# Kernel tuning notes

Hardware: AMD Instinct MI355X
Metric: run time of the kernel (lower is better)

The kernel has to match this reference:

```python
import jax, jax.numpy as jnp
import numpy as np

BN_EPS = 1e-5


def setup_inputs() -> dict:
    key = jax.random.key(0)
    ks = jax.random.split(key, 4)
    B, N, D = 8, 8192, 256
    outD = 256
    s = 1.0 / np.sqrt(D)
    return {
        "feature": jax.random.normal(ks[0], (B, N, D), dtype=jnp.float32),
        "W_qk": jax.random.normal(ks[1], (2, D, D), dtype=jnp.float32) * s,
        "b_qk": jnp.zeros((2, D), dtype=jnp.float32),
        "W_v": jax.random.normal(ks[2], (D, outD), dtype=jnp.float32) * s,
        "b_v": jnp.zeros((outD,), dtype=jnp.float32),
        "gamma": jnp.ones((D,), dtype=jnp.float32),
        "beta": jnp.zeros((D,), dtype=jnp.float32),
    }


def reference(feature, W_qk, b_qk, W_v, b_v, gamma, beta):
    # QK: [B, 2, N, D]
    QK = jnp.einsum("bnd,kde->bkne", feature, W_qk) + b_qk[None, :, None, :]
    # value: [B, N, outD]
    value = jnp.einsum("bnd,de->bne", feature, W_v) + b_v
    query = QK[:, 0]  # [B, N, D]
    key = QK[:, 1]    # [B, N, D]
    # softmax over the sequence axis (dim=1), per (batch, channel)
    sm = jax.nn.softmax(key, axis=1)
    # lambda context: softmax^T @ value -> [B, D, outD]
    lam = jnp.einsum("bnd,bne->bde", sm, value)
    # BatchNorm1d(featureDim) in training mode: channel axis = D (axis 1),
    # stats over (batch, spatial) = axes (0, 2); biased variance as torch uses.
    mean = jnp.mean(lam, axis=(0, 2), keepdims=True)
    var = jnp.var(lam, axis=(0, 2), keepdims=True)
    bn = (lam - mean) * jax.lax.rsqrt(var + BN_EPS)
    bn = bn * gamma[None, :, None] + beta[None, :, None]
    # result: query @ BN -> [B, N, outD]
    return jnp.einsum("bnd,bde->bne", query, bn)
```

## Files before the change

### kernel.cpp

```cpp
#include <hip/hip_runtime.h>

typedef unsigned short u16;
typedef __bf16 bf16x8 __attribute__((ext_vector_type(8)));
typedef float f32x4 __attribute__((ext_vector_type(4)));

#define LOG2E 1.44269504088896f

__device__ inline u16 f2b(float f) {
    unsigned u = __float_as_uint(f);
    u += 0x7fff + ((u >> 16) & 1);
    return (u16)(u >> 16);
}
__device__ inline float b2f(u16 u) { return __uint_as_float(((unsigned)u) << 16); }
__device__ inline unsigned pk2(float a, float b) {
    return (unsigned)f2b(a) | ((unsigned)f2b(b) << 16);
}
__device__ inline uint4 pack8(float4 a, float4 b) {
    return uint4{pk2(a.x, a.y), pk2(a.z, a.w), pk2(b.x, b.y), pk2(b.z, b.w)};
}
__device__ inline f32x4 mfma_bf16(uint4 a, uint4 b, f32x4 c) {
    return __builtin_amdgcn_mfma_f32_16x16x32_bf16(
        __builtin_bit_cast(bf16x8, a), __builtin_bit_cast(bf16x8, b), c, 0, 0, 0);
}
__device__ inline void ld16(const u16* g, u16* l) {
    __builtin_amdgcn_global_load_lds(
        (const __attribute__((address_space(1))) unsigned int*)g,
        (__attribute__((address_space(3))) unsigned int*)l, 16, 0, 0);
}
__device__ inline uint4 expfrag(uint4 v, float nc) {
    float e[8];
#pragma unroll
    for (int i = 0; i < 4; ++i) {
        unsigned u = ((const unsigned*)&v)[i];
        e[2 * i] = exp2f(fmaf(b2f((u16)(u & 0xffff)), LOG2E, nc));
        e[2 * i + 1] = exp2f(fmaf(b2f((u16)(u >> 16)), LOG2E, nc));
    }
    uint4 r;
    asm("v_cvt_pk_bf16_f32 %0, %1, %2" : "=v"(r.x) : "v"(e[0]), "v"(e[1]));
    asm("v_cvt_pk_bf16_f32 %0, %1, %2" : "=v"(r.y) : "v"(e[2]), "v"(e[3]));
    asm("v_cvt_pk_bf16_f32 %0, %1, %2" : "=v"(r.z) : "v"(e[4]), "v"(e[5]));
    asm("v_cvt_pk_bf16_f32 %0, %1, %2" : "=v"(r.w) : "v"(e[6]), "v"(e[7]));
    return r;
}


__global__ __launch_bounds__(256) void prep_w(const float* __restrict__ Wqk,
                                              const float* __restrict__ Wv,
                                              u16* __restrict__ WkT,
                                              u16* __restrict__ WvT,
                                              u16* __restrict__ Wqb) {
    int idx = blockIdx.x * 256 + threadIdx.x;
    int which = idx >> 16;
    int i = (idx >> 8) & 255;
    int j = idx & 255;
    if (which == 0)
        WkT[i * 256 + j] = f2b(Wqk[65536 + j * 256 + i]);
    else if (which == 1)
        WvT[i * 256 + j] = f2b(Wv[j * 256 + i]);
    else
        Wqb[i * 256 + j] = f2b(Wqk[i * 256 + j]);
}

__global__ __launch_bounds__(256, 2) void gemm_kv(const float* __restrict__ A,
                                                  const u16* __restrict__ BtK,
                                                  const u16* __restrict__ BtV,
                                                  const float* __restrict__ biasK,
                                                  const float* __restrict__ biasV,
                                                  u16* __restrict__ KT,
                                                  u16* __restrict__ VT,
                                                  float* __restrict__ partial) {
    __shared__ __align__(16) u16 lds[36864];

    const int t = threadIdx.x;
    const int r0 = blockIdx.x * 64;
    const int w = t >> 6, lane = t & 63, l15 = lane & 15, q = lane >> 4;
    const int sq = ((lane & 3) ^ ((lane >> 3) & 3)) * 8;
    const int qs = (q ^ ((l15 >> 1) & 3)) * 8;
    const int awoff = (t >> 2) * 32 + sq;
    const int brr = t >> 2;

    f32x4 accK[4][4], accV[4][4];
#pragma unroll
    for (int rt = 0; rt < 4; ++rt)
#pragma unroll
        for (int ct = 0; ct < 4; ++ct) {
            accK[rt][ct] = f32x4{0.f, 0.f, 0.f, 0.f};
            accV[rt][ct] = f32x4{0.f, 0.f, 0.f, 0.f};
        }

    const float* Arow = A + (long)(r0 + brr) * 256 + (t & 3) * 8;
    float4 p0 = ((const float4*)Arow)[0], p1 = ((const float4*)Arow)[1];
    float4 c0_ = *(const float4*)(Arow + 32), c1_ = *(const float4*)(Arow + 36);
    float4 d0_ = *(const float4*)(Arow + 64), d1_ = *(const float4*)(Arow + 68);

    {
        u16* dK = lds + 4096 + w * 512;
#pragma unroll
        for (int j = 0; j < 4; ++j) {
            int br = j * 64 + brr;
            ld16(BtK + br * 256 + sq, dK + j * 2048);
            ld16(BtV + br * 256 + sq, dK + 8192 + j * 2048);
        }
    }
    *(uint4*)(lds + awoff) = pack8(p0, p1);
    __syncthreads();

#pragma unroll
    for (int t8 = 0; t8 < 8; ++t8) {
        const int cur = t8 & 1;
        if (t8 < 7) {
            const int k0 = (t8 + 1) * 32;
            u16* dK = lds + 4096 + (cur ^ 1) * 16384 + w * 512;
#pragma unroll
            for (int j = 0; j < 4; ++j) {
                int br = j * 64 + brr;
                ld16(BtK + br * 256 + k0 + sq, dK + j * 2048);
                ld16(BtV + br * 256 + k0 + sq, dK + 8192 + j * 2048);
            }
            *(uint4*)(lds + (cur ^ 1) * 2048 + awoff) = pack8(c0_, c1_);
            c0_ = d0_; c1_ = d1_;
            if (t8 < 5) {
                d0_ = *(const float4*)(Arow + (t8 + 3) * 32);
                d1_ = *(const float4*)(Arow + (t8 + 3) * 32 + 4);
            }
        }
        const u16* Asc = lds + cur * 2048;
        const u16* Bc = lds + 4096 + cur * 16384;
        uint4 af[4];
#pragma unroll
        for (int rt = 0; rt < 4; ++rt)
            af[rt] = *(const uint4*)(Asc + (rt * 16 + l15) * 32 + qs);
#pragma unroll
        for (int ct = 0; ct < 4; ++ct) {
            const int bo = (w * 64 + ct * 16 + l15) * 32 + qs;
            uint4 bK = *(const uint4*)(Bc + bo);
            uint4 bV = *(const uint4*)(Bc + 8192 + bo);
#pragma unroll
            for (int rt = 0; rt < 4; ++rt) {
                accK[rt][ct] = mfma_bf16(af[rt], bK, accK[rt][ct]);
                accV[rt][ct] = mfma_bf16(af[rt], bV, accV[rt][ct]);
            }
        }
        __syncthreads();
    }

    const int bb = r0 >> 13;
    const int nt0 = (r0 & 8191) >> 5;
    const int nch = nt0 >> 1;
    u16* Ct = lds;
#pragma unroll
    for (int pass = 0; pass < 2; ++pass) {
        const f32x4(*acc)[4] = pass ? accV : accK;
        const float* bias = pass ? biasV : biasK;
        u16* CT = pass ? VT : KT;
#pragma unroll
        for (int ct = 0; ct < 4; ++ct) {
            const int col = w * 64 + ct * 16 + l15;
            const float bv = bias[col];
            ushort4 pks[4];
#pragma unroll
            for (int rt = 0; rt < 4; ++rt) {
                ushort4 pk;
                pk.x = f2b(acc[rt][ct][0] + bv);
                pk.y = f2b(acc[rt][ct][1] + bv);
                pk.z = f2b(acc[rt][ct][2] + bv);
                pk.w = f2b(acc[rt][ct][3] + bv);
                pks[rt] = pk;
                *(ushort4*)&Ct[col * 72 + rt * 16 + q * 4] = pk;
            }
            if (pass == 0) {
                float zm = -1e30f;
#pragma unroll
                for (int rt = 0; rt < 4; ++rt)
                    zm = fmaxf(zm,
                               fmaxf(fmaxf(b2f(pks[rt].x), b2f(pks[rt].y)),
                                     fmaxf(b2f(pks[rt].z), b2f(pks[rt].w))));
                zm = fmaxf(zm, __shfl_xor(zm, 16, 64));
                zm = fmaxf(zm, __shfl_xor(zm, 32, 64));
                zm *= LOG2E;
                float zs = 0.f;
#pragma unroll
                for (int rt = 0; rt < 4; ++rt) {
                    zs += exp2f(fmaf(b2f(pks[rt].x), LOG2E, -zm));
                    zs += exp2f(fmaf(b2f(pks[rt].y), LOG2E, -zm));
                    zs += exp2f(fmaf(b2f(pks[rt].z), LOG2E, -zm));
                    zs += exp2f(fmaf(b2f(pks[rt].w), LOG2E, -zm));
                }
                zs += __shfl_xor(zs, 16, 64);
                zs += __shfl_xor(zs, 32, 64);
                if (q == 0) {
                    float* pp =
                        partial + (((long)(bb * 128 + nch)) * 256 + col) * 2;
                    pp[0] = zm;
                    pp[1] = zs;
                }
            }
        }
        __syncthreads();
        {
            const long tb = (((long)(bb * 256 + nt0)) * 256 + t) * 32;
#pragma unroll
            for (int j2 = 0; j2 < 2; ++j2)
#pragma unroll
                for (int g = 0; g < 4; ++g)
                    *(uint4*)(CT + tb + j2 * 8192 + g * 8) =
                        *(const uint4*)&Ct[t * 72 + j2 * 32 + g * 8];
        }
        __syncthreads();
    }
}

__global__ __launch_bounds__(256) void stats2(const float* __restrict__ partial,
                                              float* __restrict__ ctab) {
    const int b = blockIdx.x, dg = blockIdx.y;
    const int t = threadIdx.x;
    const int d = dg * 32 + (t & 31);
    const int ci = t >> 5;
    float m = -1e30f, sum = 0.f;
#pragma unroll 4
    for (int k = 0; k < 16; ++k) {
        int i = ci * 16 + k;
        const float* pp = partial + (((long)(b * 128 + i)) * 256 + d) * 2;
        float mi = pp[0], si = pp[1];
        float M = fmaxf(m, mi);
        sum = sum * exp2f(m - M) + si * exp2f(mi - M);
        m = M;
    }
    __shared__ float red[512];
    red[t] = m;
    red[t + 256] = sum;
    __syncthreads();
    if (ci == 0) {
#pragma unroll
        for (int j = 1; j < 8; ++j) {
            float mi = red[t + j * 32], si = red[t + 256 + j * 32];
            float M = fmaxf(m, mi);
            sum = sum * exp2f(m - M) + si * exp2f(mi - M);
            m = M;
        }
        ctab[b * 256 + d] = m + log2f(sum);
    }
}

__global__ __launch_bounds__(256, 3) void gemm_out(const float* __restrict__ A,
                                                   const u16* __restrict__ WfoldT,
                                                   const float* __restrict__ outb,
                                                   float* __restrict__ C) {
    __shared__ __align__(16) u16 lds[20480];
    const int t = threadIdx.x;
    const int r0 = blockIdx.x * 64;
    const int bb = r0 >> 13;
    const int w = t >> 6, lane = t & 63, l15 = lane & 15, q = lane >> 4;
    const int sq = ((lane & 3) ^ ((lane >> 3) & 3)) * 8;
    const int qs = (q ^ ((l15 >> 1) & 3)) * 8;
    const int awoff = (t >> 2) * 32 + sq;
    const int brr = t >> 2;
    const u16* Bt = WfoldT + (long)bb * 65536;

    f32x4 acc[4][4];
#pragma unroll
    for (int rt = 0; rt < 4; ++rt)
#pragma unroll
        for (int ct = 0; ct < 4; ++ct) acc[rt][ct] = f32x4{0.f, 0.f, 0.f, 0.f};

    const float* Arow = A + (long)(r0 + brr) * 256 + (t & 3) * 8;
    float4 p0 = ((const float4*)Arow)[0], p1 = ((const float4*)Arow)[1];
    float4 c0_ = *(const float4*)(Arow + 32), c1_ = *(const float4*)(Arow + 36);
    float4 d0_ = *(const float4*)(Arow + 64), d1_ = *(const float4*)(Arow + 68);

    {
        u16* dB = lds + 4096 + w * 512;
#pragma unroll
        for (int j = 0; j < 4; ++j)
            ld16(Bt + (j * 64 + brr) * 256 + sq, dB + j * 2048);
    }
    *(uint4*)(lds + awoff) = pack8(p0, p1);
    __syncthreads();

#pragma unroll
    for (int t8 = 0; t8 < 8; ++t8) {
        const int cur = t8 & 1;
        if (t8 < 7) {
            const int k0 = (t8 + 1) * 32;
            u16* dB = lds + 4096 + (cur ^ 1) * 8192 + w * 512;
#pragma unroll
            for (int j = 0; j < 4; ++j)
                ld16(Bt + (j * 64 + brr) * 256 + k0 + sq, dB + j * 2048);
            *(uint4*)(lds + (cur ^ 1) * 2048 + awoff) = pack8(c0_, c1_);
            c0_ = d0_; c1_ = d1_;
            if (t8 < 5) {
                d0_ = *(const float4*)(Arow + (t8 + 3) * 32);
                d1_ = *(const float4*)(Arow + (t8 + 3) * 32 + 4);
            }
        }
        const u16* Asc = lds + cur * 2048;
        const u16* Bc = lds + 4096 + cur * 8192;
        uint4 af[4];
#pragma unroll
        for (int rt = 0; rt < 4; ++rt)
            af[rt] = *(const uint4*)(Asc + (rt * 16 + l15) * 32 + qs);
#pragma unroll
        for (int ct = 0; ct < 4; ++ct) {
            uint4 bf = *(const uint4*)(Bc + (w * 64 + ct * 16 + l15) * 32 + qs);
#pragma unroll
            for (int rt = 0; rt < 4; ++rt)
                acc[rt][ct] = mfma_bf16(af[rt], bf, acc[rt][ct]);
        }
        __syncthreads();
    }

#pragma unroll
    for (int ct = 0; ct < 4; ++ct) {
        const int col = w * 64 + ct * 16 + l15;
        const float bv = outb[bb * 256 + col];
#pragma unroll
        for (int rt = 0; rt < 4; ++rt) {
            const long rbase = r0 + rt * 16 + q * 4;
#pragma unroll
            for (int r = 0; r < 4; ++r)
                C[(rbase + r) * 256 + col] = acc[rt][ct][r] + bv;
        }
    }
}

__global__ __launch_bounds__(512, 2) void gemm_lam(const u16* __restrict__ VT,
                                                   const u16* __restrict__ KT,
                                                   const float* __restrict__ ctab,
                                                   float* __restrict__ lamP,
                                                   int nk) {
    __shared__ __align__(16) u16 lds[32768];
    const int t = threadIdx.x;
    const int b = blockIdx.x;
    const int s = blockIdx.y;
    const int w = t >> 6, lane = t & 63, l15 = lane & 15, q = lane >> 4;
    const int eg = w >> 2, dg = w & 3;
    const int sq = ((lane & 3) ^ ((lane >> 3) & 3)) * 8;
    const int qs = (q ^ ((l15 >> 1) & 3)) * 8;

    const int nt0 = s * nk;
    const u16* Vb = VT + ((long)(b * 256 + nt0)) * 8192;
    const u16* Kb = KT + ((long)(b * 256 + nt0)) * 8192;

    float nc[4];
#pragma unroll
    for (int ct = 0; ct < 4; ++ct)
        nc[ct] = -ctab[b * 256 + dg * 64 + ct * 16 + l15];

    f32x4 acc[8][4];
#pragma unroll
    for (int rt = 0; rt < 8; ++rt)
#pragma unroll
        for (int ct = 0; ct < 4; ++ct) acc[rt][ct] = f32x4{0.f, 0.f, 0.f, 0.f};

#define STAGE_TILE(tile, buf)                                                  \
    {                                                                          \
        _Pragma("unroll") for (int j = 0; j < 2; ++j) {                        \
            int g = j * 512 + t;                                               \
            ld16((tile) + (g >> 2) * 32 + sq, (buf) + (j * 512 + w * 64) * 8); \
        }                                                                      \
    }

    STAGE_TILE(Vb, lds)
    STAGE_TILE(Kb, lds + 8192)
    __syncthreads();

    for (int ks = 0; ks < nk; ++ks) {
        const int cur = ks & 1;
        if (ks + 1 < nk) {
            const u16* Vn = Vb + (long)(ks + 1) * 8192;
            const u16* Kn = Kb + (long)(ks + 1) * 8192;
            u16* dst = lds + (cur ^ 1) * 16384;
            STAGE_TILE(Vn, dst)
            STAGE_TILE(Kn, dst + 8192)
        }
        const u16* Vs = lds + cur * 16384;
        const u16* Ks = Vs + 8192;
        uint4 bf[4];
#pragma unroll
        for (int ct = 0; ct < 4; ++ct)
            bf[ct] = expfrag(
                *(const uint4*)(Ks + (dg * 64 + ct * 16 + l15) * 32 + qs),
                nc[ct]);
#pragma unroll
        for (int rt = 0; rt < 8; ++rt) {
            uint4 af = *(const uint4*)(Vs + (eg * 128 + rt * 16 + l15) * 32 + qs);
#pragma unroll
            for (int ct = 0; ct < 4; ++ct)
                acc[rt][ct] = mfma_bf16(af, bf[ct], acc[rt][ct]);
        }
        __syncthreads();
    }
#undef STAGE_TILE

    float* outp = lamP + (long)s * 524288 + (long)b * 65536;
#pragma unroll
    for (int rt = 0; rt < 8; ++rt)
#pragma unroll
        for (int ct = 0; ct < 4; ++ct) {
            const int col = dg * 64 + ct * 16 + l15;
            const int row = eg * 128 + rt * 16 + q * 4;
#pragma unroll
            for (int r = 0; r < 4; ++r)
                outp[(long)(row + r) * 256 + col] = acc[rt][ct][r];
        }
}

__global__ __launch_bounds__(256) void reduce_lam(const float* __restrict__ lamP,
                                                  float* __restrict__ lamT, int S) {
    int i = blockIdx.x * 256 + threadIdx.x;
    float4 v = ((const float4*)lamP)[i];
    for (int s = 1; s < S; ++s) {
        float4 p = ((const float4*)(lamP + (long)s * 524288))[i];
        v.x += p.x; v.y += p.y; v.z += p.z; v.w += p.w;
    }
    ((float4*)lamT)[i] = v;
}

__global__ __launch_bounds__(256, 4) void gemm_fold(const u16* __restrict__ Abn,
                                                    const u16* __restrict__ Wqb,
                                                    u16* __restrict__ WfoldT) {
    __shared__ __align__(16) u16 lds[4096];
    u16* As = lds;
    u16* Bs = lds + 2048;

    const int t = threadIdx.x;
    const int r0 = blockIdx.x * 64;
    const int c0 = blockIdx.y * 64;
    const int w = t >> 6, lane = t & 63, l15 = lane & 15, q = lane >> 4;

    f32x4 acc[4];
#pragma unroll
    for (int c = 0; c < 4; ++c) acc[c] = f32x4{0.f, 0.f, 0.f, 0.f};

    const int br = t >> 2;
    const int bk = (t & 3) * 8;

    for (int k0 = 0; k0 < 256; k0 += 32) {
        ld16(Abn + (long)(r0 + br) * 256 + k0 + bk, As + w * 512);
        ld16(Wqb + (long)(c0 + br) * 256 + k0 + bk, Bs + w * 512);
        __syncthreads();
        uint4 af = *(const uint4*)(As + (w * 16 + l15) * 32 + q * 8);
#pragma unroll
        for (int c = 0; c < 4; ++c) {
            uint4 bf = *(const uint4*)(Bs + (c * 16 + l15) * 32 + q * 8);
            acc[c] = mfma_bf16(af, bf, acc[c]);
        }
        __syncthreads();
    }

#pragma unroll
    for (int c = 0; c < 4; ++c) {
        int col = c0 + c * 16 + l15;
#pragma unroll
        for (int r = 0; r < 4; ++r) {
            int row = r0 + w * 16 + q * 4 + r;
            WfoldT[(long)row * 256 + col] = f2b(acc[c][r]);
        }
    }
}

__global__ __launch_bounds__(256) void bn_kernel(const float* __restrict__ lamT,
                                                 const float* __restrict__ gamma,
                                                 const float* __restrict__ beta,
                                                 u16* __restrict__ bnT) {
    const int d = blockIdx.x;
    const int t = threadIdx.x;
    float vals[8];
    float s = 0.f, ss = 0.f;
#pragma unroll
    for (int i = 0; i < 8; ++i) {
        float v = lamT[(long)(i * 256 + t) * 256 + d];
        vals[i] = v;
        s += v;
        ss += v * v;
    }
#pragma unroll
    for (int sh = 32; sh > 0; sh >>= 1) {
        s += __shfl_xor(s, sh, 64);
        ss += __shfl_xor(ss, sh, 64);
    }
    __shared__ float red[8];
    int w = t >> 6;
    if ((t & 63) == 0) {
        red[w] = s;
        red[w + 4] = ss;
    }
    __syncthreads();
    s = red[0] + red[1] + red[2] + red[3];
    ss = red[4] + red[5] + red[6] + red[7];
    float mean = s * (1.f / 2048.f);
    float var = ss * (1.f / 2048.f) - mean * mean;
    float scale = gamma[d] * rsqrtf(var + 1e-5f);
    float shift = beta[d] - mean * scale;
#pragma unroll
    for (int i = 0; i < 8; ++i)
        bnT[(long)(i * 256 + t) * 256 + d] = f2b(vals[i] * scale + shift);
}

__global__ __launch_bounds__(256) void outb_kernel(const float* __restrict__ bq,
                                                   const u16* __restrict__ bnT,
                                                   float* __restrict__ outb) {
    int b = blockIdx.x, e = threadIdx.x;
    const u16* rowp = bnT + ((long)b * 256 + e) * 256;
    float s = 0.f;
    for (int dd = 0; dd < 256; ++dd) s += bq[dd] * b2f(rowp[dd]);
    outb[b * 256 + e] = s;
}

extern "C" void kernel_launch(void* const* d_in, const int* in_sizes, int n_in,
                              void* d_out, int out_size, void* d_ws, size_t ws_size,
                              hipStream_t stream) {
    const float* feat = (const float*)d_in[0];
    const float* W_qk = (const float*)d_in[1];
    const float* b_qk = (const float*)d_in[2];
    const float* W_v = (const float*)d_in[3];
    const float* b_v = (const float*)d_in[4];
    const float* gamma = (const float*)d_in[5];
    const float* beta = (const float*)d_in[6];
    float* out = (float*)d_out;

    char* ws = (char*)d_ws;
    u16* KT = (u16*)(ws);
    u16* VT = (u16*)(ws + 33554432);
    u16* WkT = (u16*)(ws + 67108864);
    u16* WvT = (u16*)(ws + 67239936);
    u16* Wqb = (u16*)(ws + 67371008);
    float* partial = (float*)(ws + 67502080);
    float* ctab = (float*)(ws + 69599232);
    const size_t base = 69607424;
    float* lamP = (float*)(ws + base);
    size_t avail = (ws_size > base) ? ws_size - base : 0;
    int S = (avail >= 16u * 2097152u) ? 16
          : (avail >= 8u * 2097152u) ? 8
          : (avail >= 4u * 2097152u) ? 4 : 2;
    float* lamT = (float*)ws;
    u16* bnT = (u16*)(ws + 2097152);
    u16* WfoldT = (u16*)(ws + 3145728);
    float* outb = (float*)(ws + 4194304);

    prep_w<<<768, 256, 0, stream>>>(W_qk, W_v, WkT, WvT, Wqb);
    gemm_kv<<<1024, 256, 0, stream>>>(feat, WkT, WvT, b_qk + 256, b_v, KT, VT,
                                      partial);
    stats2<<<dim3(8, 8), 256, 0, stream>>>(partial, ctab);
    gemm_lam<<<dim3(8, S), 512, 0, stream>>>(VT, KT, ctab, lamP, 8192 / S / 32);
    reduce_lam<<<512, 256, 0, stream>>>(lamP, lamT, S);
    bn_kernel<<<256, 256, 0, stream>>>(lamT, gamma, beta, bnT);
    outb_kernel<<<8, 256, 0, stream>>>(b_qk, bnT, outb);
    gemm_fold<<<dim3(32, 4), 256, 0, stream>>>(bnT, Wqb, WfoldT);
    gemm_out<<<1024, 256, 0, stream>>>(feat, WfoldT, outb, out);
}
```

Before: 261.1 us.

## Split gemm_kv across 8 waves per matrix, retile gemm_lam into smaller blocks

gemm_kv now runs with 512 threads. Each wave computes only K or only V for a 64-column group, and the kernel drops double buffering to single-buffer smaller LDS, which should raise occupancy and lower register pressure. gemm_lam is retiled from 8 large blocks per split into 64 blocks of 64x128 outputs with 256 threads. The number of splits is capped at 8, which gives more blocks with less per-block work and a smaller partial-sum reduction. In exchange, gemm_kv loses its global-to-LDS prefetch overlap, and gemm_lam rereads V/K tiles across blocks, raising L2 traffic.

```diff
diff --git a/kernel.cpp b/kernel.cpp
--- a/kernel.cpp
+++ b/kernel.cpp
@@ -12,12 +12,6 @@
     return (u16)(u >> 16);
 }
 __device__ inline float b2f(u16 u) { return __uint_as_float(((unsigned)u) << 16); }
-__device__ inline unsigned pk2(float a, float b) {
-    return (unsigned)f2b(a) | ((unsigned)f2b(b) << 16);
-}
-__device__ inline uint4 pack8(float4 a, float4 b) {
-    return uint4{pk2(a.x, a.y), pk2(a.z, a.w), pk2(b.x, b.y), pk2(b.z, b.w)};
-}
 __device__ inline f32x4 mfma_bf16(uint4 a, uint4 b, f32x4 c) {
     return __builtin_amdgcn_mfma_f32_16x16x32_bf16(
         __builtin_bit_cast(bf16x8, a), __builtin_bit_cast(bf16x8, b), c, 0, 0, 0);
@@ -61,7 +55,7 @@
         Wqb[i * 256 + j] = f2b(Wqk[i * 256 + j]);
 }
 
-__global__ __launch_bounds__(256, 2) void gemm_kv(const float* __restrict__ A,
+__global__ __launch_bounds__(512, 4) void gemm_kv(const float* __restrict__ A,
                                                   const u16* __restrict__ BtK,
                                                   const u16* __restrict__ BtV,
                                                   const float* __restrict__ biasK,
@@ -69,77 +63,48 @@
                                                   u16* __restrict__ KT,
                                                   u16* __restrict__ VT,
                                                   float* __restrict__ partial) {
-    __shared__ __align__(16) u16 lds[36864];
+    __shared__ __align__(16) u16 lds[18432];
 
     const int t = threadIdx.x;
     const int r0 = blockIdx.x * 64;
     const int w = t >> 6, lane = t & 63, l15 = lane & 15, q = lane >> 4;
+    const int mat = w & 1, cg = w >> 1;
     const int sq = ((lane & 3) ^ ((lane >> 3) & 3)) * 8;
     const int qs = (q ^ ((l15 >> 1) & 3)) * 8;
-    const int awoff = (t >> 2) * 32 + sq;
-    const int brr = t >> 2;
-
-    f32x4 accK[4][4], accV[4][4];
+    const int arow = t >> 3;
+    const int aq = ((t & 7) >> 1) ^ ((arow >> 1) & 3);
+    const int awoff = arow * 32 + aq * 8 + (t & 1) * 4;
+    const float* Ap = A + (long)(r0 + arow) * 256 + (t & 7) * 4;
+    const u16* Bs = lds + 2048 + mat * 8192;
+
+    f32x4 acc[4][4];
 #pragma unroll
     for (int rt = 0; rt < 4; ++rt)
 #pragma unroll
+        for (int ct = 0; ct < 4; ++ct) acc[rt][ct] = f32x4{0.f, 0.f, 0.f, 0.f};
+
+    float4 a = *(const float4*)Ap;
+    for (int ks = 0; ks < 8; ++ks) {
+        const int k0 = ks * 32;
+#pragma unroll
+        for (int j = 0; j < 2; ++j) {
+            const int src = (j * 128 + (t >> 2)) * 256 + k0 + sq;
+            ld16(BtK + src, lds + 2048 + j * 4096 + w * 512);
+            ld16(BtV + src, lds + 10240 + j * 4096 + w * 512);
+        }
+        *(ushort4*)&lds[awoff] = ushort4{f2b(a.x), f2b(a.y), f2b(a.z), f2b(a.w)};
+        __syncthreads();
+        if (ks < 7) a = *(const float4*)(Ap + k0 + 32);
+        uint4 af[4];
+#pragma unroll
+        for (int rt = 0; rt < 4; ++rt)
+            af[rt] = *(const uint4*)(lds + (rt * 16 + l15) * 32 + qs);
+#pragma unroll
         for (int ct = 0; ct < 4; ++ct) {
-            accK[rt][ct] = f32x4{0.f, 0.f, 0.f, 0.f};
-            accV[rt][ct] = f32x4{0.f, 0.f, 0.f, 0.f};
-        }
-
-    const float* Arow = A + (long)(r0 + brr) * 256 + (t & 3) * 8;
-    float4 p0 = ((const float4*)Arow)[0], p1 = ((const float4*)Arow)[1];
-    float4 c0_ = *(const float4*)(Arow + 32), c1_ = *(const float4*)(Arow + 36);
-    float4 d0_ = *(const float4*)(Arow + 64), d1_ = *(const float4*)(Arow + 68);
-
-    {
-        u16* dK = lds + 4096 + w * 512;
-#pragma unroll
-        for (int j = 0; j < 4; ++j) {
-            int br = j * 64 + brr;
-            ld16(BtK + br * 256 + sq, dK + j * 2048);
-            ld16(BtV + br * 256 + sq, dK + 8192 + j * 2048);
-        }
-    }
-    *(uint4*)(lds + awoff) = pack8(p0, p1);
-    __syncthreads();
-
-#pragma unroll
-    for (int t8 = 0; t8 < 8; ++t8) {
-        const int cur = t8 & 1;
-        if (t8 < 7) {
-            const int k0 = (t8 + 1) * 32;
-            u16* dK = lds + 4096 + (cur ^ 1) * 16384 + w * 512;
-#pragma unroll
-            for (int j = 0; j < 4; ++j) {
-                int br = j * 64 + brr;
-                ld16(BtK + br * 256 + k0 + sq, dK + j * 2048);
-                ld16(BtV + br * 256 + k0 + sq, dK + 8192 + j * 2048);
-            }
-            *(uint4*)(lds + (cur ^ 1) * 2048 + awoff) = pack8(c0_, c1_);
-            c0_ = d0_; c1_ = d1_;
-            if (t8 < 5) {
-                d0_ = *(const float4*)(Arow + (t8 + 3) * 32);
-                d1_ = *(const float4*)(Arow + (t8 + 3) * 32 + 4);
-            }
-        }
-        const u16* Asc = lds + cur * 2048;
-        const u16* Bc = lds + 4096 + cur * 16384;
-        uint4 af[4];
-#pragma unroll
-        for (int rt = 0; rt < 4; ++rt)
-            af[rt] = *(const uint4*)(Asc + (rt * 16 + l15) * 32 + qs);
-#pragma unroll
-        for (int ct = 0; ct < 4; ++ct) {
-            const int bo = (w * 64 + ct * 16 + l15) * 32 + qs;
-            uint4 bK = *(const uint4*)(Bc + bo);
-            uint4 bV = *(const uint4*)(Bc + 8192 + bo);
-#pragma unroll
-            for (int rt = 0; rt < 4; ++rt) {
-                accK[rt][ct] = mfma_bf16(af[rt], bK, accK[rt][ct]);
-                accV[rt][ct] = mfma_bf16(af[rt], bV, accV[rt][ct]);
-            }
+            uint4 bf = *(const uint4*)(Bs + (cg * 64 + ct * 16 + l15) * 32 + qs);
+#pragma unroll
+            for (int rt = 0; rt < 4; ++rt)
+                acc[rt][ct] = mfma_bf16(af[rt], bf, acc[rt][ct]);
         }
         __syncthreads();
     }
@@ -147,64 +112,63 @@
     const int bb = r0 >> 13;
     const int nt0 = (r0 & 8191) >> 5;
     const int nch = nt0 >> 1;
-    u16* Ct = lds;
+    const float* bias = mat ? biasV : biasK;
 #pragma unroll
     for (int pass = 0; pass < 2; ++pass) {
-        const f32x4(*acc)[4] = pass ? accV : accK;
-        const float* bias = pass ? biasV : biasK;
-        u16* CT = pass ? VT : KT;
-#pragma unroll
-        for (int ct = 0; ct < 4; ++ct) {
-            const int col = w * 64 + ct * 16 + l15;
-            const float bv = bias[col];
-            ushort4 pks[4];
-#pragma unroll
-            for (int rt = 0; rt < 4; ++rt) {
-                ushort4 pk;
-                pk.x = f2b(acc[rt][ct][0] + bv);
-                pk.y = f2b(acc[rt][ct][1] + bv);
-                pk.z = f2b(acc[rt][ct][2] + bv);
-                pk.w = f2b(acc[rt][ct][3] + bv);
-                pks[rt] = pk;
-                *(ushort4*)&Ct[col * 72 + rt * 16 + q * 4] = pk;
-            }
-            if (pass == 0) {
-                float zm = -1e30f;
-#pragma unroll
-                for (int rt = 0; rt < 4; ++rt)
-                    zm = fmaxf(zm,
-                               fmaxf(fmaxf(b2f(pks[rt].x), b2f(pks[rt].y)),
-                                     fmaxf(b2f(pks[rt].z), b2f(pks[rt].w))));
-                zm = fmaxf(zm, __shfl_xor(zm, 16, 64));
-                zm = fmaxf(zm, __shfl_xor(zm, 32, 64));
-                zm *= LOG2E;
-                float zs = 0.f;
+        if (mat == pass) {
+#pragma unroll
+            for (int ct = 0; ct < 4; ++ct) {
+                const int col = cg * 64 + ct * 16 + l15;
+                const float bv = bias[col];
+                ushort4 pks[4];
 #pragma unroll
                 for (int rt = 0; rt < 4; ++rt) {
-                    zs += exp2f(fmaf(b2f(pks[rt].x), LOG2E, -zm));
-                    zs += exp2f(fmaf(b2f(pks[rt].y), LOG2E, -zm));
-                    zs += exp2f(fmaf(b2f(pks[rt].z), LOG2E, -zm));
-                    zs += exp2f(fmaf(b2f(pks[rt].w), LOG2E, -zm));
+                    ushort4 pk;
+                    pk.x = f2b(acc[rt][ct][0] + bv);
+                    pk.y = f2b(acc[rt][ct][1] + bv);
+                    pk.z = f2b(acc[rt][ct][2] + bv);
+                    pk.w = f2b(acc[rt][ct][3] + bv);
+                    pks[rt] = pk;
+                    *(ushort4*)&lds[col * 72 + rt * 16 + q * 4] = pk;
                 }
-                zs += __shfl_xor(zs, 16, 64);
-                zs += __shfl_xor(zs, 32, 64);
-                if (q == 0) {
-                    float* pp =
-                        partial + (((long)(bb * 128 + nch)) * 256 + col) * 2;
-                    pp[0] = zm;
-                    pp[1] = zs;
+                if (pass == 0) {
+                    float zm = -1e30f;
+#pragma unroll
+                    for (int rt = 0; rt < 4; ++rt)
+                        zm = fmaxf(zm,
+                                   fmaxf(fmaxf(b2f(pks[rt].x), b2f(pks[rt].y)),
+                                         fmaxf(b2f(pks[rt].z), b2f(pks[rt].w))));
+                    zm = fmaxf(zm, __shfl_xor(zm, 16, 64));
+                    zm = fmaxf(zm, __shfl_xor(zm, 32, 64));
+                    zm *= LOG2E;
+                    float zs = 0.f;
+#pragma unroll
+                    for (int rt = 0; rt < 4; ++rt) {
+                        zs += exp2f(fmaf(b2f(pks[rt].x), LOG2E, -zm));
+                        zs += exp2f(fmaf(b2f(pks[rt].y), LOG2E, -zm));
+                        zs += exp2f(fmaf(b2f(pks[rt].z), LOG2E, -zm));
+                        zs += exp2f(fmaf(b2f(pks[rt].w), LOG2E, -zm));
+                    }
+                    zs += __shfl_xor(zs, 16, 64);
+                    zs += __shfl_xor(zs, 32, 64);
+                    if (q == 0) {
+                        float* pp =
+                            partial + (((long)(bb * 128 + nch)) * 256 + col) * 2;
+                        pp[0] = zm;
+                        pp[1] = zs;
+                    }
                 }
             }
         }
         __syncthreads();
         {
-            const long tb = (((long)(bb * 256 + nt0)) * 256 + t) * 32;
-#pragma unroll
-            for (int j2 = 0; j2 < 2; ++j2)
-#pragma unroll
-                for (int g = 0; g < 4; ++g)
-                    *(uint4*)(CT + tb + j2 * 8192 + g * 8) =
-                        *(const uint4*)&Ct[t * 72 + j2 * 32 + g * 8];
+            u16* CT = pass ? VT : KT;
+            const int d = t >> 1, j2 = t & 1;
+            const long dst = (((long)(bb * 256 + nt0 + j2)) * 256 + d) * 32;
+#pragma unroll
+            for (int g = 0; g < 4; ++g)
+                *(uint4*)(CT + dst + g * 8) =
+                    *(const uint4*)&lds[d * 72 + j2 * 32 + g * 8];
         }
         __syncthreads();
     }
@@ -274,7 +238,12 @@
         for (int j = 0; j < 4; ++j)
             ld16(Bt + (j * 64 + brr) * 256 + sq, dB + j * 2048);
     }
-    *(uint4*)(lds + awoff) = pack8(p0, p1);
+    {
+        ushort4 lo{f2b(p0.x), f2b(p0.y), f2b(p0.z), f2b(p0.w)};
+        ushort4 hi{f2b(p1.x), f2b(p1.y), f2b(p1.z), f2b(p1.w)};
+        *(ushort4*)&lds[awoff] = lo;
+        *(ushort4*)&lds[awoff + 4] = hi;
+    }
     __syncthreads();
 
 #pragma unroll
@@ -286,7 +255,10 @@
 #pragma unroll
             for (int j = 0; j < 4; ++j)
                 ld16(Bt + (j * 64 + brr) * 256 + k0 + sq, dB + j * 2048);
-            *(uint4*)(lds + (cur ^ 1) * 2048 + awoff) = pack8(c0_, c1_);
+            ushort4 lo{f2b(c0_.x), f2b(c0_.y), f2b(c0_.z), f2b(c0_.w)};
+            ushort4 hi{f2b(c1_.x), f2b(c1_.y), f2b(c1_.z), f2b(c1_.w)};
+            *(ushort4*)&lds[(cur ^ 1) * 2048 + awoff] = lo;
+            *(ushort4*)&lds[(cur ^ 1) * 2048 + awoff + 4] = hi;
             c0_ = d0_; c1_ = d1_;
             if (t8 < 5) {
                 d0_ = *(const float4*)(Arow + (t8 + 3) * 32);
@@ -323,45 +295,37 @@
     }
 }
 
-__global__ __launch_bounds__(512, 2) void gemm_lam(const u16* __restrict__ VT,
+__global__ __launch_bounds__(256, 6) void gemm_lam(const u16* __restrict__ VT,
                                                    const u16* __restrict__ KT,
                                                    const float* __restrict__ ctab,
                                                    float* __restrict__ lamP,
                                                    int nk) {
-    __shared__ __align__(16) u16 lds[32768];
+    __shared__ __align__(16) u16 lds[12288];
     const int t = threadIdx.x;
-    const int b = blockIdx.x;
+    const int bx = blockIdx.x;
+    const int b = bx >> 3, e0 = ((bx >> 1) & 3) * 64, d0 = (bx & 1) * 128;
     const int s = blockIdx.y;
     const int w = t >> 6, lane = t & 63, l15 = lane & 15, q = lane >> 4;
-    const int eg = w >> 2, dg = w & 3;
     const int sq = ((lane & 3) ^ ((lane >> 3) & 3)) * 8;
     const int qs = (q ^ ((l15 >> 1) & 3)) * 8;
 
-    const int nt0 = s * nk;
-    const u16* Vb = VT + ((long)(b * 256 + nt0)) * 8192;
-    const u16* Kb = KT + ((long)(b * 256 + nt0)) * 8192;
-
-    float nc[4];
-#pragma unroll
-    for (int ct = 0; ct < 4; ++ct)
-        nc[ct] = -ctab[b * 256 + dg * 64 + ct * 16 + l15];
-
-    f32x4 acc[8][4];
-#pragma unroll
-    for (int rt = 0; rt < 8; ++rt)
-#pragma unroll
-        for (int ct = 0; ct < 4; ++ct) acc[rt][ct] = f32x4{0.f, 0.f, 0.f, 0.f};
-
-#define STAGE_TILE(tile, buf)                                                  \
-    {                                                                          \
-        _Pragma("unroll") for (int j = 0; j < 2; ++j) {                        \
-            int g = j * 512 + t;                                               \
-            ld16((tile) + (g >> 2) * 32 + sq, (buf) + (j * 512 + w * 64) * 8); \
-        }                                                                      \
-    }
-
-    STAGE_TILE(Vb, lds)
-    STAGE_TILE(Kb, lds + 8192)
+    const long nt0 = (long)s * nk;
+    const u16* Vb = VT + ((long)b * 256 + nt0) * 8192;
+    const u16* Kb = KT + ((long)b * 256 + nt0) * 8192;
+
+    float nc0 = -ctab[b * 256 + d0 + w * 32 + l15];
+    float nc1 = -ctab[b * 256 + d0 + w * 32 + 16 + l15];
+
+    f32x4 acc[4][2];
+#pragma unroll
+    for (int rt = 0; rt < 4; ++rt) {
+        acc[rt][0] = f32x4{0.f, 0.f, 0.f, 0.f};
+        acc[rt][1] = f32x4{0.f, 0.f, 0.f, 0.f};
+    }
+
+    ld16(Vb + (e0 + (t >> 2)) * 32 + sq, lds + w * 512);
+    ld16(Kb + (d0 + (t >> 2)) * 32 + sq, lds + 2048 + w * 512);
+    ld16(Kb + (d0 + 64 + (t >> 2)) * 32 + sq, lds + 4096 + w * 512);
     __syncthreads();
 
     for (int ks = 0; ks < nk; ++ks) {
@@ -369,36 +333,32 @@
         if (ks + 1 < nk) {
             const u16* Vn = Vb + (long)(ks + 1) * 8192;
             const u16* Kn = Kb + (long)(ks + 1) * 8192;
-            u16* dst = lds + (cur ^ 1) * 16384;
-            STAGE_TILE(Vn, dst)
-            STAGE_TILE(Kn, dst + 8192)
-        }
-        const u16* Vs = lds + cur * 16384;
-        const u16* Ks = Vs + 8192;
-        uint4 bf[4];
-#pragma unroll
-        for (int ct = 0; ct < 4; ++ct)
-            bf[ct] = expfrag(
-                *(const uint4*)(Ks + (dg * 64 + ct * 16 + l15) * 32 + qs),
-                nc[ct]);
-#pragma unroll
-        for (int rt = 0; rt < 8; ++rt) {
-            uint4 af = *(const uint4*)(Vs + (eg * 128 + rt * 16 + l15) * 32 + qs);
-#pragma unroll
-            for (int ct = 0; ct < 4; ++ct)
-                acc[rt][ct] = mfma_bf16(af, bf[ct], acc[rt][ct]);
-        }
-        __syncthreads();
-    }
-#undef STAGE_TILE
+            u16* dst = lds + (cur ^ 1) * 6144;
+            ld16(Vn + (e0 + (t >> 2)) * 32 + sq, dst + w * 512);
+            ld16(Kn + (d0 + (t >> 2)) * 32 + sq, dst + 2048 + w * 512);
+            ld16(Kn + (d0 + 64 + (t >> 2)) * 32 + sq, dst + 4096 + w * 512);
+        }
+        const u16* Vs = lds + cur * 6144;
+        const u16* Ks = Vs + 2048;
+        uint4 bf0 = expfrag(*(const uint4*)(Ks + (w * 32 + l15) * 32 + qs), nc0);
+        uint4 bf1 =
+            expfrag(*(const uint4*)(Ks + (w * 32 + 16 + l15) * 32 + qs), nc1);
+#pragma unroll
+        for (int rt = 0; rt < 4; ++rt) {
+            uint4 af = *(const uint4*)(Vs + (rt * 16 + l15) * 32 + qs);
+            acc[rt][0] = mfma_bf16(af, bf0, acc[rt][0]);
+            acc[rt][1] = mfma_bf16(af, bf1, acc[rt][1]);
+        }
+        __syncthreads();
+    }
 
     float* outp = lamP + (long)s * 524288 + (long)b * 65536;
 #pragma unroll
-    for (int rt = 0; rt < 8; ++rt)
-#pragma unroll
-        for (int ct = 0; ct < 4; ++ct) {
-            const int col = dg * 64 + ct * 16 + l15;
-            const int row = eg * 128 + rt * 16 + q * 4;
+    for (int rt = 0; rt < 4; ++rt)
+#pragma unroll
+        for (int ct = 0; ct < 2; ++ct) {
+            const int col = d0 + w * 32 + ct * 16 + l15;
+            const int row = e0 + rt * 16 + q * 4;
 #pragma unroll
             for (int r = 0; r < 4; ++r)
                 outp[(long)(row + r) * 256 + col] = acc[rt][ct][r];
@@ -530,8 +490,7 @@
     const size_t base = 69607424;
     float* lamP = (float*)(ws + base);
     size_t avail = (ws_size > base) ? ws_size - base : 0;
-    int S = (avail >= 16u * 2097152u) ? 16
-          : (avail >= 8u * 2097152u) ? 8
+    int S = (avail >= 8u * 2097152u) ? 8
           : (avail >= 4u * 2097152u) ? 4 : 2;
     float* lamT = (float*)ws;
     u16* bnT = (u16*)(ws + 2097152);
@@ -539,10 +498,10 @@
     float* outb = (float*)(ws + 4194304);
 
     prep_w<<<768, 256, 0, stream>>>(W_qk, W_v, WkT, WvT, Wqb);
-    gemm_kv<<<1024, 256, 0, stream>>>(feat, WkT, WvT, b_qk + 256, b_v, KT, VT,
+    gemm_kv<<<1024, 512, 0, stream>>>(feat, WkT, WvT, b_qk + 256, b_v, KT, VT,
                                       partial);
     stats2<<<dim3(8, 8), 256, 0, stream>>>(partial, ctab);
-    gemm_lam<<<dim3(8, S), 512, 0, stream>>>(VT, KT, ctab, lamP, 8192 / S / 32);
+    gemm_lam<<<dim3(64, S), 256, 0, stream>>>(VT, KT, ctab, lamP, 8192 / (S * 32));
     reduce_lam<<<512, 256, 0, stream>>>(lamP, lamT, S);
     bn_kernel<<<256, 256, 0, stream>>>(lamT, gamma, beta, bnT);
     outb_kernel<<<8, 256, 0, stream>>>(b_qk, bnT, outb);
```

Measured after the change: 257.4 us. No clear change (-1.4%).
